# Performance work log

Hardware: AMD Instinct MI355X
Metric: run time of the kernel (lower is better)

Reference implementation:

```python
import jax, jax.numpy as jnp
import numpy as np

K = 512           # num_embeddings
D = 256           # embedding_dim
GRID = (16, 32)   # SOM grid, prod == K
SIGMA = 2.0       # Gaussian neighborhood width (blur at step 0)
COMMITMENT_COST = 0.25
KOHONEN_COST = 1.0


def _make_blur_matrix():
    # Grid.init id->coord: coord[j] = (i // prod(shape[:j])) % shape[j]
    idx = np.arange(K)
    c0 = idx % GRID[0]
    c1 = (idx // GRID[0]) % GRID[1]
    coords = np.stack([c0, c1], axis=-1).astype(np.float32)  # [K, 2]
    dist = np.linalg.norm(coords[None, :, :] - coords[:, None, :], axis=-1)  # [K, K]
    return jnp.asarray(np.exp(-(dist ** 2) / (2.0 * SIGMA ** 2)), dtype=jnp.float32)


def setup_inputs() -> dict:
    key = jax.random.key(0)
    kx, kw = jax.random.split(key)
    x = jax.random.normal(kx, (64, 32, 32, D), dtype=jnp.float32)
    w = jax.random.normal(kw, (K, D), dtype=jnp.float32)
    bmat = _make_blur_matrix()  # [K, K] constant buffer
    return {"x": x, "w": w, "bmat": bmat}


def reference(x, w, bmat):
    sg = jax.lax.stop_gradient
    flat = x.reshape(-1, D)  # [N, D]

    # nearest-code search (no_grad in torch)
    fw = sg(flat)
    ww = sg(w)
    dists = (jnp.sum(fw ** 2, axis=1, keepdims=True)
             + jnp.sum(ww ** 2, axis=1)
             - 2.0 * fw @ ww.T)                       # [N, K]
    enc_idx = jnp.argmin(dists, axis=1)               # [N]
    encodings = jax.nn.one_hot(enc_idx, K, dtype=jnp.float32)  # [N, K]

    # embedding lookup (differentiable w.r.t. w)
    quant_flat = w[enc_idx]                           # [N, D]
    quantized = quant_flat.reshape(x.shape)

    # l2_batch(w, quantized.detach()) -> [N, K]
    qd = sg(quant_flat)
    diff = (jnp.sum(w ** 2, axis=1)[None, :]
            + jnp.sum(qd ** 2, axis=1, keepdims=True)
            - 2.0 * qd @ w.T)                         # [N, K]

    # blur-weighted kohonen loss: bmm(diff[N,1,K], bmat[idx][N,K,1]).mean()
    selected = bmat[enc_idx]                          # [N, K]
    kohonen_loss = jnp.mean(jnp.sum(diff * selected, axis=-1))

    avg_probs = jnp.mean(encodings, axis=0)
    perplexity = jnp.exp(-jnp.sum(avg_probs * jnp.log(avg_probs + 1e-10)))

    e_latent = jnp.mean((sg(quantized) - x) ** 2)
    q_latent = jnp.mean((quantized - sg(x)) ** 2)
    loss = q_latent + COMMITMENT_COST * e_latent + KOHONEN_COST * kohonen_loss

    quantized_st = x + sg(quantized - x)              # straight-through
    return loss, quantized_st, perplexity, enc_idx
```

## Files before the change

kernel.cpp:

```cpp
#include <hip/hip_runtime.h>
#include <hip/hip_bf16.h>
#include <hip/hip_fp16.h>
#include <math.h>

#define NPTS 65536
#define DIM  256
#define KC   512

#define BM    64
#define NBLK  (NPTS / BM)
#define XSTR  264
#define EPS   0.05f

#define QOFF  1
#define PIDX  16777217
#define EOFF  16777218


typedef _Float16 h8    __attribute__((ext_vector_type(8)));
typedef float    f32x4 __attribute__((ext_vector_type(4)));

__device__ inline void cvt_split8(float4 a, float4 b, h8& hv, h8& lv) {
    float f[8] = {a.x, a.y, a.z, a.w, b.x, b.y, b.z, b.w};
    #pragma unroll
    for (int i = 0; i < 8; ++i) {
        _Float16 h = (_Float16)f[i];
        hv[i] = h;
        lv[i] = (_Float16)(f[i] - (float)h);
    }
}

__device__ inline void merge_top2(float& b1, int& i1, float& b2, int& i2,
                                  float ob1, int oi1, float ob2, int oi2) {
    bool ow = (ob1 < b1) || (ob1 == b1 && oi1 < i1);
    float lb = ow ? b1 : ob1; int li = ow ? i1 : oi1;
    if (ow) { b1 = ob1; i1 = oi1; }
    float c2 = b2; int ci = i2;
    if (ob2 < c2 || (ob2 == c2 && oi2 < ci)) { c2 = ob2; ci = oi2; }
    if (lb  < c2 || (lb  == c2 && li  < ci)) { c2 = lb;  ci = li;  }
    b2 = c2; i2 = ci;
}

__device__ inline float exact_dist(const float* __restrict__ xr,
                                   const float* __restrict__ w, int c, float wsqc) {
    const float* wr = w + (size_t)c * DIM;
    float d0 = 0.f, d1 = 0.f, d2 = 0.f, d3 = 0.f;
    #pragma unroll 4
    for (int d = 0; d < DIM; d += 4) {
        d0 = fmaf(xr[d + 0], wr[d + 0], d0);
        d1 = fmaf(xr[d + 1], wr[d + 1], d1);
        d2 = fmaf(xr[d + 2], wr[d + 2], d2);
        d3 = fmaf(xr[d + 3], wr[d + 3], d3);
    }
    return wsqc - 2.f * ((d0 + d1) + (d2 + d3));
}

__global__ __launch_bounds__(256) void som_prep(const float* __restrict__ w,
                                                _Float16* __restrict__ wfh,
                                                _Float16* __restrict__ wfl,
                                                float* __restrict__ wsq,
                                                int* __restrict__ hist,
                                                double* __restrict__ mse_acc)
{
    int c = blockIdx.x * 256 + threadIdx.x;
    const float4* r = reinterpret_cast<const float4*>(w + (size_t)c * DIM);

    float s0 = 0.f, s1 = 0.f, s2 = 0.f, s3 = 0.f;
    #pragma unroll 8
    for (int q = 0; q < DIM / 4; ++q) {
        float4 v = r[q];
        s0 = fmaf(v.x, v.x, s0);
        s1 = fmaf(v.y, v.y, s1);
        s2 = fmaf(v.z, v.z, s2);
        s3 = fmaf(v.w, v.w, s3);
    }
    wsq[c] = (s0 + s1) + (s2 + s3);
    hist[c] = 0;
    if (c == 0) *mse_acc = 0.0;

    int ctg = c >> 4, l15 = c & 15;
    #pragma unroll 4
    for (int g = 0; g < 32; ++g) {
        float4 a = r[g * 2], b = r[g * 2 + 1];
        h8 hv, lv; cvt_split8(a, b, hv, lv);
        int dsl = g >> 2, kg = g & 3;
        size_t off = (((size_t)(ctg * 8 + dsl)) * 4 + kg) * 128 + l15 * 8;
        *reinterpret_cast<h8*>(wfh + off) = hv;
        *reinterpret_cast<h8*>(wfl + off) = lv;
    }
}

__global__ __launch_bounds__(256) void som_main(const float* __restrict__ x,
                                                const float* __restrict__ w,
                                                const _Float16* __restrict__ wfh,
                                                const _Float16* __restrict__ wfl,
                                                float* __restrict__ out,
                                                const float* __restrict__ wsq,
                                                int* __restrict__ hist,
                                                double* __restrict__ mse_acc)
{
    alignas(16) __shared__ _Float16 xh[BM * XSTR];
    alignas(16) __shared__ _Float16 xl[BM * XSTR];
    __shared__ float wsq_s[KC];
    __shared__ float red_b[4][BM], red_s[4][BM];
    __shared__ int   red_ib[4][BM], red_is[4][BM];
    __shared__ int   bidx_s[BM];
    __shared__ float wsum[4];

    const int tid  = threadIdx.x;
    const int lane = tid & 63;
    const int wid  = tid >> 6;
    const int l15  = lane & 15;
    const int kg   = lane >> 4;
    const int ptBlock = blockIdx.x * BM;

    const float4* xg4 = reinterpret_cast<const float4*>(x);
    #pragma unroll
    for (int it = 0; it < 8; ++it) {
        int u = it * 256 + tid;
        int row = u >> 5, c8 = u & 31;
        float4 a = xg4[(size_t)(ptBlock + row) * 64 + c8 * 2];
        float4 b = xg4[(size_t)(ptBlock + row) * 64 + c8 * 2 + 1];
        h8 hv, lv; cvt_split8(a, b, hv, lv);
        *reinterpret_cast<h8*>(&xh[row * XSTR + c8 * 8]) = hv;
        *reinterpret_cast<h8*>(&xl[row * XSTR + c8 * 8]) = lv;
    }
    wsq_s[tid] = wsq[tid];
    wsq_s[256 + tid] = wsq[256 + tid];
    __syncthreads();

    float sb[4], ss[4];
    int   ib[4], is2[4];
    #pragma unroll
    for (int ct = 0; ct < 4; ++ct) { sb[ct] = INFINITY; ss[ct] = INFINITY; ib[ct] = 0; is2[ct] = 0; }

    const int codeBase = wid * 128;

    #pragma unroll 1
    for (int pass = 0; pass < 2; ++pass) {
        f32x4 acc[4][4];
        #pragma unroll
        for (int rt = 0; rt < 4; ++rt)
            #pragma unroll
            for (int ct = 0; ct < 4; ++ct)
                acc[rt][ct] = (f32x4){0.f, 0.f, 0.f, 0.f};

        #pragma unroll 1
        for (int dsl = 0; dsl < 8; ++dsl) {
            h8 Bh[4], Bl[4];
            #pragma unroll
            for (int ct = 0; ct < 4; ++ct) {
                int off = (ct * 16 + l15) * XSTR + dsl * 32 + kg * 8;
                Bh[ct] = *reinterpret_cast<const h8*>(&xh[off]);
                Bl[ct] = *reinterpret_cast<const h8*>(&xl[off]);
            }
            #pragma unroll
            for (int rt = 0; rt < 4; ++rt) {
                int ctg = (codeBase >> 4) + pass * 4 + rt;
                size_t off = (((size_t)ctg * 8 + dsl) * 4 + kg) * 128 + l15 * 8;
                h8 Ah = *reinterpret_cast<const h8*>(wfh + off);
                h8 Al = *reinterpret_cast<const h8*>(wfl + off);
                #pragma unroll
                for (int ct = 0; ct < 4; ++ct) {
                    acc[rt][ct] = __builtin_amdgcn_mfma_f32_16x16x32_f16(Ah, Bh[ct], acc[rt][ct], 0, 0, 0);
                    acc[rt][ct] = __builtin_amdgcn_mfma_f32_16x16x32_f16(Al, Bh[ct], acc[rt][ct], 0, 0, 0);
                    acc[rt][ct] = __builtin_amdgcn_mfma_f32_16x16x32_f16(Ah, Bl[ct], acc[rt][ct], 0, 0, 0);
                }
            }
        }

        #pragma unroll
        for (int rt = 0; rt < 4; ++rt) {
            int cbase = codeBase + pass * 64 + rt * 16 + kg * 4;
            #pragma unroll
            for (int ct = 0; ct < 4; ++ct) {
                #pragma unroll
                for (int r = 0; r < 4; ++r) {
                    int c = cbase + r;
                    float d = wsq_s[c] - 2.f * acc[rt][ct][r];
                    if (d < sb[ct] || (d == sb[ct] && c < ib[ct])) {
                        ss[ct] = sb[ct]; is2[ct] = ib[ct]; sb[ct] = d; ib[ct] = c;
                    } else if (d < ss[ct] || (d == ss[ct] && c < is2[ct])) {
                        ss[ct] = d; is2[ct] = c;
                    }
                }
            }
        }
    }

    #pragma unroll
    for (int ct = 0; ct < 4; ++ct) {
        #pragma unroll
        for (int m = 16; m <= 32; m <<= 1) {
            float ob1 = __shfl_xor(sb[ct], m, 64), ob2 = __shfl_xor(ss[ct], m, 64);
            int   oi1 = __shfl_xor(ib[ct], m, 64), oi2 = __shfl_xor(is2[ct], m, 64);
            merge_top2(sb[ct], ib[ct], ss[ct], is2[ct], ob1, oi1, ob2, oi2);
        }
    }
    if (kg == 0) {
        #pragma unroll
        for (int ct = 0; ct < 4; ++ct) {
            int p = ct * 16 + l15;
            red_b[wid][p] = sb[ct];  red_s[wid][p] = ss[ct];
            red_ib[wid][p] = ib[ct]; red_is[wid][p] = is2[ct];
        }
    }
    __syncthreads();

    if (tid < BM) {
        float b = red_b[0][tid], s = red_s[0][tid];
        int  bi = red_ib[0][tid], si = red_is[0][tid];
        #pragma unroll
        for (int g = 1; g < 4; ++g)
            merge_top2(b, bi, s, si, red_b[g][tid], red_ib[g][tid], red_s[g][tid], red_is[g][tid]);

        if (s - b < EPS) {
            const float* xr = x + (size_t)(ptBlock + tid) * DIM;
            float d1 = exact_dist(xr, w, bi, wsq_s[bi]);
            float d2 = exact_dist(xr, w, si, wsq_s[si]);
            if (d2 < d1 || (d2 == d1 && si < bi)) bi = si;
        }
        bidx_s[tid] = bi;
        out[EOFF + ptBlock + tid] = (float)bi;
        atomicAdd(&hist[bi], 1);
    }
    __syncthreads();

    float lsum = 0.f;
    for (int p = 0; p < BM; ++p) {
        int c = bidx_s[p];
        float qv = w[(size_t)c * DIM + tid];
        float xv = x[(size_t)(ptBlock + p) * DIM + tid];
        out[QOFF + (size_t)(ptBlock + p) * DIM + tid] = qv;
        float dd = qv - xv;
        lsum = fmaf(dd, dd, lsum);
    }
    #pragma unroll
    for (int m = 32; m; m >>= 1) lsum += __shfl_xor(lsum, m, 64);
    if (lane == 0) wsum[wid] = lsum;
    __syncthreads();
    if (tid == 0)
        atomicAdd(mse_acc, (double)((wsum[0] + wsum[1]) + (wsum[2] + wsum[3])));
}

__global__ __launch_bounds__(256) void som_g(const float* __restrict__ w,
                                             const float* __restrict__ bmat,
                                             const float* __restrict__ wsq,
                                             float* __restrict__ g)
{
    __shared__ float wj[DIM];
    __shared__ float psum[4];
    const int j = blockIdx.x;
    const int tid = threadIdx.x;
    wj[tid] = w[(size_t)j * DIM + tid];
    __syncthreads();
    const float wsqj = wsq[j];
    float sum = 0.f;
    for (int k = tid; k < KC; k += 256) {
        const float* wk = &w[(size_t)k * DIM];
        float d0 = 0.f, d1 = 0.f, d2 = 0.f, d3 = 0.f;
        #pragma unroll 4
        for (int d = 0; d < DIM; d += 4) {
            d0 = fmaf(wj[d + 0], wk[d + 0], d0);
            d1 = fmaf(wj[d + 1], wk[d + 1], d1);
            d2 = fmaf(wj[d + 2], wk[d + 2], d2);
            d3 = fmaf(wj[d + 3], wk[d + 3], d3);
        }
        float dot = (d0 + d1) + (d2 + d3);
        float t = wsq[k] + wsqj - 2.f * dot;
        sum = fmaf(bmat[(size_t)j * KC + k], t, sum);
    }
    #pragma unroll
    for (int m = 32; m; m >>= 1) sum += __shfl_xor(sum, m, 64);
    int lane = tid & 63, wid = tid >> 6;
    if (lane == 0) psum[wid] = sum;
    __syncthreads();
    if (tid == 0) g[j] = (psum[0] + psum[1]) + (psum[2] + psum[3]);
}

__global__ __launch_bounds__(512) void som_final(const int* __restrict__ hist,
                                                 const float* __restrict__ g,
                                                 const double* __restrict__ mse_acc,
                                                 float* __restrict__ out)
{
    __shared__ float e_part[8], k_part[8];
    const int tid = threadIdx.x;
    int cnt = hist[tid];
    float p = (float)cnt / (float)NPTS;
    float ent = -p * logf(p + 1e-10f);
    float koh = (float)cnt * g[tid];
    #pragma unroll
    for (int m = 32; m; m >>= 1) {
        ent += __shfl_xor(ent, m, 64);
        koh += __shfl_xor(koh, m, 64);
    }
    int lane = tid & 63, wid = tid >> 6;
    if (lane == 0) { e_part[wid] = ent; k_part[wid] = koh; }
    __syncthreads();
    if (tid == 0) {
        float es = 0.f, ks = 0.f;
        #pragma unroll
        for (int i = 0; i < 8; ++i) { es += e_part[i]; ks += k_part[i]; }
        float mse = (float)(*mse_acc / (double)(NPTS * (size_t)DIM));
        out[0] = fmaf(1.25f, mse, ks / (float)NPTS);
        out[PIDX] = expf(es);
    }
}

extern "C" void kernel_launch(void* const* d_in, const int* in_sizes, int n_in,
                              void* d_out, int out_size, void* d_ws, size_t ws_size,
                              hipStream_t stream) {
    const float* x    = (const float*)d_in[0];
    const float* w    = (const float*)d_in[1];
    const float* bmat = (const float*)d_in[2];
    float* out = (float*)d_out;

    _Float16* wfh = (_Float16*)d_ws;
    _Float16* wfl = wfh + 131072;
    float*  wsq  = (float*)((char*)d_ws + 524288);
    float*  g    = (float*)((char*)d_ws + 526336);
    int*    hist = (int*)((char*)d_ws + 528384);
    double* mse  = (double*)((char*)d_ws + 530432);

    som_prep <<<2, 256, 0, stream>>>(w, wfh, wfl, wsq, hist, mse);
    som_main <<<NBLK, 256, 0, stream>>>(x, w, wfh, wfl, out, wsq, hist, mse);
    som_g    <<<KC, 256, 0, stream>>>(w, bmat, wsq, g);
    som_final<<<1, KC, 0, stream>>>(hist, g, mse, out);
}
```

Baseline: 193.5 us.

## Use 8 waves per block over codes, split weight prep, tighten rescoring margin

```diff
diff --git a/kernel.cpp b/kernel.cpp
--- a/kernel.cpp
+++ b/kernel.cpp
@@ -10,7 +10,7 @@
 #define BM    64
 #define NBLK  (NPTS / BM)
 #define XSTR  264
-#define EPS   0.05f
+#define EPS   0.01f
 
 #define QOFF  1
 #define PIDX  16777217
@@ -55,16 +55,13 @@
     return wsqc - 2.f * ((d0 + d1) + (d2 + d3));
 }
 
-__global__ __launch_bounds__(256) void som_prep(const float* __restrict__ w,
-                                                _Float16* __restrict__ wfh,
-                                                _Float16* __restrict__ wfl,
-                                                float* __restrict__ wsq,
-                                                int* __restrict__ hist,
-                                                double* __restrict__ mse_acc)
-{
-    int c = blockIdx.x * 256 + threadIdx.x;
-    const float4* r = reinterpret_cast<const float4*>(w + (size_t)c * DIM);
-
+__global__ __launch_bounds__(256) void som_wsq(const float* __restrict__ w,
+                                               float* __restrict__ wsq,
+                                               int* __restrict__ hist,
+                                               double* __restrict__ mse_acc)
+{
+    int k = blockIdx.x * 256 + threadIdx.x;
+    const float4* r = reinterpret_cast<const float4*>(w + (size_t)k * DIM);
     float s0 = 0.f, s1 = 0.f, s2 = 0.f, s3 = 0.f;
     #pragma unroll 8
     for (int q = 0; q < DIM / 4; ++q) {
@@ -74,23 +71,29 @@
         s2 = fmaf(v.z, v.z, s2);
         s3 = fmaf(v.w, v.w, s3);
     }
-    wsq[c] = (s0 + s1) + (s2 + s3);
-    hist[c] = 0;
-    if (c == 0) *mse_acc = 0.0;
-
-    int ctg = c >> 4, l15 = c & 15;
-    #pragma unroll 4
-    for (int g = 0; g < 32; ++g) {
-        float4 a = r[g * 2], b = r[g * 2 + 1];
-        h8 hv, lv; cvt_split8(a, b, hv, lv);
-        int dsl = g >> 2, kg = g & 3;
-        size_t off = (((size_t)(ctg * 8 + dsl)) * 4 + kg) * 128 + l15 * 8;
-        *reinterpret_cast<h8*>(wfh + off) = hv;
-        *reinterpret_cast<h8*>(wfl + off) = lv;
-    }
-}
-
-__global__ __launch_bounds__(256) void som_main(const float* __restrict__ x,
+    wsq[k] = (s0 + s1) + (s2 + s3);
+    hist[k] = 0;
+    if (k == 0) *mse_acc = 0.0;
+}
+
+__global__ __launch_bounds__(256) void som_conv(const float* __restrict__ w,
+                                                _Float16* __restrict__ wfh,
+                                                _Float16* __restrict__ wfl)
+{
+    const int tid = threadIdx.x;
+    const int row = blockIdx.x * 8 + (tid >> 5);
+    const int g   = tid & 31;
+    const float4* r = reinterpret_cast<const float4*>(w + (size_t)row * DIM);
+    float4 a = r[g * 2], b = r[g * 2 + 1];
+    h8 hv, lv; cvt_split8(a, b, hv, lv);
+    int dsl = g >> 2, kg = g & 3;
+    int ctg = row >> 4, l15 = row & 15;
+    size_t off = (((size_t)(ctg * 8 + dsl)) * 4 + kg) * 128 + l15 * 8;
+    *reinterpret_cast<h8*>(wfh + off) = hv;
+    *reinterpret_cast<h8*>(wfl + off) = lv;
+}
+
+__global__ __launch_bounds__(512) void som_main(const float* __restrict__ x,
                                                 const float* __restrict__ w,
                                                 const _Float16* __restrict__ wfh,
                                                 const _Float16* __restrict__ wfl,
@@ -102,10 +105,10 @@
     alignas(16) __shared__ _Float16 xh[BM * XSTR];
     alignas(16) __shared__ _Float16 xl[BM * XSTR];
     __shared__ float wsq_s[KC];
-    __shared__ float red_b[4][BM], red_s[4][BM];
-    __shared__ int   red_ib[4][BM], red_is[4][BM];
+    __shared__ float red_b[8][BM], red_s[8][BM];
+    __shared__ int   red_ib[8][BM], red_is[8][BM];
     __shared__ int   bidx_s[BM];
-    __shared__ float wsum[4];
+    __shared__ float wsum[8];
 
     const int tid  = threadIdx.x;
     const int lane = tid & 63;
@@ -116,8 +119,8 @@
 
     const float4* xg4 = reinterpret_cast<const float4*>(x);
     #pragma unroll
-    for (int it = 0; it < 8; ++it) {
-        int u = it * 256 + tid;
+    for (int it = 0; it < 4; ++it) {
+        int u = it * 512 + tid;
         int row = u >> 5, c8 = u & 31;
         float4 a = xg4[(size_t)(ptBlock + row) * 64 + c8 * 2];
         float4 b = xg4[(size_t)(ptBlock + row) * 64 + c8 * 2 + 1];
@@ -126,7 +129,6 @@
         *reinterpret_cast<h8*>(&xl[row * XSTR + c8 * 8]) = lv;
     }
     wsq_s[tid] = wsq[tid];
-    wsq_s[256 + tid] = wsq[256 + tid];
     __syncthreads();
 
     float sb[4], ss[4];
@@ -134,55 +136,55 @@
     #pragma unroll
     for (int ct = 0; ct < 4; ++ct) { sb[ct] = INFINITY; ss[ct] = INFINITY; ib[ct] = 0; is2[ct] = 0; }
 
-    const int codeBase = wid * 128;
+    const int codeBase = wid * 64;
+
+    f32x4 acc[4][4];
+    #pragma unroll
+    for (int rt = 0; rt < 4; ++rt)
+        #pragma unroll
+        for (int ct = 0; ct < 4; ++ct)
+            acc[rt][ct] = (f32x4){0.f, 0.f, 0.f, 0.f};
 
     #pragma unroll 1
-    for (int pass = 0; pass < 2; ++pass) {
-        f32x4 acc[4][4];
-        #pragma unroll
-        for (int rt = 0; rt < 4; ++rt)
+    for (int dsl = 0; dsl < 8; ++dsl) {
+        h8 Bh[4], Bl[4];
+        #pragma unroll
+        for (int ct = 0; ct < 4; ++ct) {
+            int off = (ct * 16 + l15) * XSTR + dsl * 32 + kg * 8;
+            Bh[ct] = *reinterpret_cast<const h8*>(&xh[off]);
+            Bl[ct] = *reinterpret_cast<const h8*>(&xl[off]);
+        }
+        #pragma unroll
+        for (int rt = 0; rt < 4; ++rt) {
+            int ctg = (codeBase >> 4) + rt;
+            size_t off = (((size_t)ctg * 8 + dsl) * 4 + kg) * 128 + l15 * 8;
+            h8 Ah = *reinterpret_cast<const h8*>(wfh + off);
+            h8 Al = *reinterpret_cast<const h8*>(wfl + off);
             #pragma unroll
             for (int ct = 0; ct < 4; ++ct)
-                acc[rt][ct] = (f32x4){0.f, 0.f, 0.f, 0.f};
-
-        #pragma unroll 1
-        for (int dsl = 0; dsl < 8; ++dsl) {
-            h8 Bh[4], Bl[4];
+                acc[rt][ct] = __builtin_amdgcn_mfma_f32_16x16x32_f16(Ah, Bh[ct], acc[rt][ct], 0, 0, 0);
             #pragma unroll
-            for (int ct = 0; ct < 4; ++ct) {
-                int off = (ct * 16 + l15) * XSTR + dsl * 32 + kg * 8;
-                Bh[ct] = *reinterpret_cast<const h8*>(&xh[off]);
-                Bl[ct] = *reinterpret_cast<const h8*>(&xl[off]);
-            }
+            for (int ct = 0; ct < 4; ++ct)
+                acc[rt][ct] = __builtin_amdgcn_mfma_f32_16x16x32_f16(Al, Bh[ct], acc[rt][ct], 0, 0, 0);
             #pragma unroll
-            for (int rt = 0; rt < 4; ++rt) {
-                int ctg = (codeBase >> 4) + pass * 4 + rt;
-                size_t off = (((size_t)ctg * 8 + dsl) * 4 + kg) * 128 + l15 * 8;
-                h8 Ah = *reinterpret_cast<const h8*>(wfh + off);
-                h8 Al = *reinterpret_cast<const h8*>(wfl + off);
-                #pragma unroll
-                for (int ct = 0; ct < 4; ++ct) {
-                    acc[rt][ct] = __builtin_amdgcn_mfma_f32_16x16x32_f16(Ah, Bh[ct], acc[rt][ct], 0, 0, 0);
-                    acc[rt][ct] = __builtin_amdgcn_mfma_f32_16x16x32_f16(Al, Bh[ct], acc[rt][ct], 0, 0, 0);
-                    acc[rt][ct] = __builtin_amdgcn_mfma_f32_16x16x32_f16(Ah, Bl[ct], acc[rt][ct], 0, 0, 0);
-                }
-            }
-        }
-
-        #pragma unroll
-        for (int rt = 0; rt < 4; ++rt) {
-            int cbase = codeBase + pass * 64 + rt * 16 + kg * 4;
+            for (int ct = 0; ct < 4; ++ct)
+                acc[rt][ct] = __builtin_amdgcn_mfma_f32_16x16x32_f16(Ah, Bl[ct], acc[rt][ct], 0, 0, 0);
+        }
+    }
+
+    #pragma unroll
+    for (int rt = 0; rt < 4; ++rt) {
+        int cbase = codeBase + rt * 16 + kg * 4;
+        #pragma unroll
+        for (int ct = 0; ct < 4; ++ct) {
             #pragma unroll
-            for (int ct = 0; ct < 4; ++ct) {
-                #pragma unroll
-                for (int r = 0; r < 4; ++r) {
-                    int c = cbase + r;
-                    float d = wsq_s[c] - 2.f * acc[rt][ct][r];
-                    if (d < sb[ct] || (d == sb[ct] && c < ib[ct])) {
-                        ss[ct] = sb[ct]; is2[ct] = ib[ct]; sb[ct] = d; ib[ct] = c;
-                    } else if (d < ss[ct] || (d == ss[ct] && c < is2[ct])) {
-                        ss[ct] = d; is2[ct] = c;
-                    }
+            for (int r = 0; r < 4; ++r) {
+                int c = cbase + r;
+                float d = wsq_s[c] - 2.f * acc[rt][ct][r];
+                if (d < sb[ct] || (d == sb[ct] && c < ib[ct])) {
+                    ss[ct] = sb[ct]; is2[ct] = ib[ct]; sb[ct] = d; ib[ct] = c;
+                } else if (d < ss[ct] || (d == ss[ct] && c < is2[ct])) {
+                    ss[ct] = d; is2[ct] = c;
                 }
             }
         }
@@ -211,7 +213,7 @@
         float b = red_b[0][tid], s = red_s[0][tid];
         int  bi = red_ib[0][tid], si = red_is[0][tid];
         #pragma unroll
-        for (int g = 1; g < 4; ++g)
+        for (int g = 1; g < 8; ++g)
             merge_top2(b, bi, s, si, red_b[g][tid], red_ib[g][tid], red_s[g][tid], red_is[g][tid]);
 
         if (s - b < EPS) {
@@ -226,21 +228,30 @@
     }
     __syncthreads();
 
-    float lsum = 0.f;
-    for (int p = 0; p < BM; ++p) {
-        int c = bidx_s[p];
-        float qv = w[(size_t)c * DIM + tid];
-        float xv = x[(size_t)(ptBlock + p) * DIM + tid];
-        out[QOFF + (size_t)(ptBlock + p) * DIM + tid] = qv;
-        float dd = qv - xv;
-        lsum = fmaf(dd, dd, lsum);
-    }
-    #pragma unroll
-    for (int m = 32; m; m >>= 1) lsum += __shfl_xor(lsum, m, 64);
-    if (lane == 0) wsum[wid] = lsum;
-    __syncthreads();
-    if (tid == 0)
-        atomicAdd(mse_acc, (double)((wsum[0] + wsum[1]) + (wsum[2] + wsum[3])));
+    {
+        int d = tid & 255;
+        int ph = tid >> 8;
+        float lsum = 0.f;
+        for (int pp = 0; pp < BM / 2; ++pp) {
+            int p = pp * 2 + ph;
+            int c = bidx_s[p];
+            float qv = w[(size_t)c * DIM + d];
+            float xv = x[(size_t)(ptBlock + p) * DIM + d];
+            out[QOFF + (size_t)(ptBlock + p) * DIM + d] = qv;
+            float dd = qv - xv;
+            lsum = fmaf(dd, dd, lsum);
+        }
+        #pragma unroll
+        for (int m = 32; m; m >>= 1) lsum += __shfl_xor(lsum, m, 64);
+        if (lane == 0) wsum[wid] = lsum;
+    }
+    __syncthreads();
+    if (tid == 0) {
+        float t = 0.f;
+        #pragma unroll
+        for (int i = 0; i < 8; ++i) t += wsum[i];
+        atomicAdd(mse_acc, (double)t);
+    }
 }
 
 __global__ __launch_bounds__(256) void som_g(const float* __restrict__ w,
@@ -322,8 +333,9 @@
     int*    hist = (int*)((char*)d_ws + 528384);
     double* mse  = (double*)((char*)d_ws + 530432);
 
-    som_prep <<<2, 256, 0, stream>>>(w, wfh, wfl, wsq, hist, mse);
-    som_main <<<NBLK, 256, 0, stream>>>(x, w, wfh, wfl, out, wsq, hist, mse);
+    som_wsq  <<<2, 256, 0, stream>>>(w, wsq, hist, mse);
+    som_conv <<<64, 256, 0, stream>>>(w, wfh, wfl);
+    som_main <<<NBLK, 512, 0, stream>>>(x, w, wfh, wfl, out, wsq, hist, mse);
     som_g    <<<KC, 256, 0, stream>>>(w, bmat, wsq, g);
     som_final<<<1, KC, 0, stream>>>(hist, g, mse, out);
 }
```

Result: faster. 163.4 us (median of 3 runs) (-15.5%).
